# Kernel tuning notes

Hardware: AMD Instinct MI355X
Metric: run time of the kernel (lower is better)

Reference implementation:

```python
import jax, jax.numpy as jnp
import numpy as np

B, S, IN_DIM, HID, H, CS = 4, 4096, 1024, 1024, 16, 16
HD = HID // H
LN_EPS = 1e-5


def setup_inputs() -> dict:
    key = jax.random.key(0)
    ks = jax.random.split(key, 6)
    x = jax.random.normal(ks[0], (B, S, IN_DIM), jnp.float32)
    W_in = jax.random.normal(ks[1], (HID, IN_DIM), jnp.float32) * (IN_DIM ** -0.5)
    ln_g = jnp.ones((HID,), jnp.float32)
    ln_b = jnp.zeros((HID,), jnp.float32)
    W_gate = jax.random.normal(ks[2], (2 * H, HID), jnp.float32) * (HID ** -0.5)
    b_gate = jnp.zeros((2 * H,), jnp.float32)
    raw = 0.5 * float(np.log(1.9 / 0.1))  # atanh(0.9), as in _init_eigenvalues
    eig_raw = jnp.full((H,), raw, jnp.float32) + 0.01 * jax.random.normal(ks[3], (H,), jnp.float32)
    W_out = jax.random.normal(ks[4], (HID, HID), jnp.float32) * (HID ** -0.5)
    return {"x": x, "W_in": W_in, "ln_g": ln_g, "ln_b": ln_b,
            "W_gate": W_gate, "b_gate": b_gate, "eig_raw": eig_raw, "W_out": W_out}


def _chunk_scan(a, b):
    # a: (B,S,H) decay, b: (B,S,H,HD) input; h_t = a_t*h_{t-1} + b_t, h0 = 0
    Bsz, Sl = a.shape[0], a.shape[1]
    N = Sl // CS  # seq_len chosen divisible by chunk_size (pad_len == 0)
    ac = a.reshape(Bsz, N, CS, H)
    bc = b.reshape(Bsz, N, CS, H, HD)
    cum = jnp.cumprod(ac, axis=2)  # (B,N,C,H)
    ones = jnp.ones((Bsz, N, 1, H), a.dtype)
    cum_pad = jnp.concatenate([ones, cum[:, :, :-1]], axis=2)  # shifted cumprod
    # M[i,j] = cum_i / cum_pad_j for i>j, 1 on diag, 0 above
    Mi = cum[:, :, :, None, :]        # (B,N,C,1,H)
    Mj = cum_pad[:, :, None, :, :]    # (B,N,1,C,H)
    M = jnp.where(jnp.abs(Mj) > 1e-8, Mi / Mj, jnp.zeros_like(Mi))
    tril = jnp.tril(jnp.ones((CS, CS), a.dtype))[None, None, :, :, None]
    eye = jnp.eye(CS, dtype=a.dtype)[None, None, :, :, None]
    M = M * tril
    M = M * (1 - eye) + eye  # force exact 1 on diagonal
    # within-chunk contribution: (B,N,C,H,HD)
    h_contrib = jnp.einsum('bnijh,bnjhd->bnihd', M, bc)
    # inter-chunk sequential carry
    cum_T = jnp.moveaxis(cum, 1, 0)            # (N,B,C,H)
    hc_T = jnp.moveaxis(h_contrib, 1, 0)       # (N,B,C,H,HD)

    def step(h, inp):
        cum_n, hc_n = inp
        h_chunk = cum_n[..., None] * h[:, None] + hc_n  # (B,C,H,HD)
        return h_chunk[:, -1], h_chunk

    h0 = jnp.zeros((Bsz, H, HD), a.dtype)
    _, h_all = jax.lax.scan(step, h0, (cum_T, hc_T))   # (N,B,C,H,HD)
    h_all = jnp.moveaxis(h_all, 0, 1).reshape(Bsz, Sl, HID)
    return h_all


def reference(x, W_in, ln_g, ln_b, W_gate, b_gate, eig_raw, W_out):
    Bsz, Sl, _ = x.shape
    xp = x @ W_in.T                               # (B,S,HID)
    mu = jnp.mean(xp, axis=-1, keepdims=True)
    var = jnp.mean((xp - mu) ** 2, axis=-1, keepdims=True)
    xp = (xp - mu) * jax.lax.rsqrt(var + LN_EPS) * ln_g + ln_b
    gates = xp @ W_gate.T + b_gate                # (B,S,2H)
    alpha = jax.nn.sigmoid(gates[..., :H])
    beta = jax.nn.sigmoid(gates[..., H:])
    eig = jnp.tanh(eig_raw)                       # (H,)
    a = eig[None, None, :] * alpha                # (B,S,H)
    x_heads = xp.reshape(Bsz, Sl, H, HD)
    b = beta[..., None] * x_heads                 # (B,S,H,HD)
    h_all = _chunk_scan(a, b)                     # (B,S,HID)
    output = h_all @ W_out.T                      # dropout is identity in eval
    h_final = h_all[:, -1, :]
    return output, h_final
```

## Files before the change

kernel.cpp:

```cpp
#include <hip/hip_runtime.h>
#include <hip/hip_bf16.h>
#include <stdint.h>

#define BATCH 4
#define SEQ   4096
#define HID   1024
#define NH    16
#define HD    64
#define CS    16
#define NCH   256
#define MROWS 16384

typedef __attribute__((ext_vector_type(8))) __bf16 bf16x8;
typedef __attribute__((ext_vector_type(4))) float  f32x4;

__device__ __forceinline__ unsigned short f2bf(float f) {
    union { float f; unsigned u; } x; x.f = f;
    unsigned r = x.u + 0x7FFFu + ((x.u >> 16) & 1u);
    return (unsigned short)(r >> 16);
}
__device__ __forceinline__ float bf2f(unsigned short v) {
    union { unsigned u; float f; } x; x.u = ((unsigned)v) << 16;
    return x.f;
}

__device__ __forceinline__ void async_copy16(void* lds, const void* g) {
    __builtin_amdgcn_global_load_lds(
        (const __attribute__((address_space(1))) unsigned int*)g,
        (__attribute__((address_space(3))) unsigned int*)lds,
        16, 0, 0);
}

__global__ __launch_bounds__(256) void convert_all_kernel(
    const float* __restrict__ x, const float* __restrict__ W_in,
    const float* __restrict__ W_out, const float* __restrict__ W_gate,
    unsigned short* __restrict__ xb, unsigned short* __restrict__ Wib,
    unsigned short* __restrict__ Wob, unsigned short* __restrict__ Wgb)
{
    int i = blockIdx.x * 256 + threadIdx.x;
    const float4* src; ushort4* dst; int j;
    if (i < 4194304)      { src = (const float4*)x;      dst = (ushort4*)xb;  j = i; }
    else if (i < 4456448) { src = (const float4*)W_in;   dst = (ushort4*)Wib; j = i - 4194304; }
    else if (i < 4718592) { src = (const float4*)W_out;  dst = (ushort4*)Wob; j = i - 4456448; }
    else if (i < 4726784) { src = (const float4*)W_gate; dst = (ushort4*)Wgb; j = i - 4718592; }
    else return;
    float4 v = src[j];
    ushort4 o;
    o.x = f2bf(v.x); o.y = f2bf(v.y); o.z = f2bf(v.z); o.w = f2bf(v.w);
    dst[j] = o;
}

__global__ __launch_bounds__(256, 2) void gemm_bt_kernel(
    const unsigned short* __restrict__ A,
    const unsigned short* __restrict__ Bm,
    float* __restrict__ C, int M, int N, int K)
{
    __shared__ unsigned short As[128 * 64];
    __shared__ unsigned short Bs[128 * 64];
    const int t = threadIdx.x;
    const int lane = t & 63, w = t >> 6;
    const int wm = w >> 1, wn = w & 1;
    const size_t bm = (size_t)blockIdx.x * 128;
    const size_t bn = (size_t)blockIdx.y * 128;

    f32x4 acc[4][4];
#pragma unroll
    for (int x = 0; x < 4; x++)
#pragma unroll
        for (int y = 0; y < 4; y++)
            acc[x][y] = (f32x4){0.f, 0.f, 0.f, 0.f};

    const int srow = lane >> 3;
    const int gc   = (lane & 7) ^ (srow & 7);
    const int scol = gc * 8;
    const unsigned short* Ag = A + (bm + w * 32 + srow) * (size_t)K + scol;
    const unsigned short* Bg = Bm + (bn + w * 32 + srow) * (size_t)K + scol;
    unsigned short* Al = As + (w * 32 + srow) * 64 + (lane & 7) * 8;
    unsigned short* Bl = Bs + (w * 32 + srow) * 64 + (lane & 7) * 8;

    const int fr = lane & 15, fq = lane >> 4;
    const int rl = fr & 7;

    for (int k0 = 0; k0 < K; k0 += 64) {
#pragma unroll
        for (int r = 0; r < 4; r++) {
            async_copy16(Al + r * 8 * 64, Ag + (size_t)r * 8 * K + k0);
            async_copy16(Bl + r * 8 * 64, Bg + (size_t)r * 8 * K + k0);
        }
        __syncthreads();
#pragma unroll
        for (int kk = 0; kk < 64; kk += 32) {
            const int c = (kk >> 3) + fq;
            const int pc = c ^ rl;
            bf16x8 af[4], bfv[4];
#pragma unroll
            for (int x = 0; x < 4; x++) {
                af[x]  = *(const bf16x8*)(As + (wm * 64 + x * 16 + fr) * 64 + pc * 8);
                bfv[x] = *(const bf16x8*)(Bs + (wn * 64 + x * 16 + fr) * 64 + pc * 8);
            }
#pragma unroll
            for (int x = 0; x < 4; x++)
#pragma unroll
                for (int y = 0; y < 4; y++)
                    acc[x][y] = __builtin_amdgcn_mfma_f32_16x16x32_bf16(af[x], bfv[y], acc[x][y], 0, 0, 0);
        }
        __syncthreads();
    }

#pragma unroll
    for (int x = 0; x < 4; x++) {
#pragma unroll
        for (int y = 0; y < 4; y++) {
            size_t r0 = bm + wm * 64 + x * 16 + fq * 4;
            size_t c  = bn + wn * 64 + y * 16 + fr;
#pragma unroll
            for (int rg = 0; rg < 4; rg++)
                C[(r0 + rg) * (size_t)N + c] = acc[x][y][rg];
        }
    }
}

__global__ __launch_bounds__(256) void mid_kernel(
    const float* __restrict__ xp,
    const float* __restrict__ ln_g, const float* __restrict__ ln_b,
    const unsigned short* __restrict__ Wgb,
    const float* __restrict__ bg, const float* __restrict__ eig_raw,
    unsigned short* __restrict__ xln,
    float* __restrict__ beta_buf,
    float* __restrict__ cum_out,
    float* __restrict__ c15c,
    float* __restrict__ hc15)
{
    __shared__ unsigned short sx[16][1032];
    __shared__ float red[4][2][64][4];
    __shared__ float sg[16][32];
    __shared__ float scum[16][16];
    const int t = threadIdx.x, lane = t & 63, w = t >> 6;
    const int bn = blockIdx.x;
    const size_t m0 = (size_t)(bn >> 8) * SEQ + (size_t)(bn & 255) * 16;

    const int r = t >> 4, u = t & 15;
    {
        const float* row = xp + (m0 + r) * 1024;
        float4 v[16];
        float s = 0.f, s2 = 0.f;
#pragma unroll
        for (int i = 0; i < 16; i++) {
            v[i] = *(const float4*)(row + u * 4 + i * 64);
            s  += v[i].x + v[i].y + v[i].z + v[i].w;
            s2 += v[i].x * v[i].x + v[i].y * v[i].y + v[i].z * v[i].z + v[i].w * v[i].w;
        }
#pragma unroll
        for (int off = 1; off < 16; off <<= 1) {
            s  += __shfl_xor(s, off, 64);
            s2 += __shfl_xor(s2, off, 64);
        }
        const float mu = s * (1.f / 1024.f);
        const float var = s2 * (1.f / 1024.f) - mu * mu;
        const float sc = rsqrtf(var + 1e-5f);
        unsigned short* orow = xln + (m0 + r) * 1024;
#pragma unroll
        for (int i = 0; i < 16; i++) {
            const int k = u * 4 + i * 64;
            float4 g4 = *(const float4*)(ln_g + k);
            float4 b4 = *(const float4*)(ln_b + k);
            ushort4 o;
            o.x = f2bf((v[i].x - mu) * sc * g4.x + b4.x);
            o.y = f2bf((v[i].y - mu) * sc * g4.y + b4.y);
            o.z = f2bf((v[i].z - mu) * sc * g4.z + b4.z);
            o.w = f2bf((v[i].w - mu) * sc * g4.w + b4.w);
            *(ushort4*)&sx[r][k] = o;
            *(ushort4*)(orow + k) = o;
        }
    }
    __syncthreads();

    const int fr = lane & 15, fq = lane >> 4;
    {
        f32x4 acc0 = (f32x4){0.f,0.f,0.f,0.f}, acc1 = (f32x4){0.f,0.f,0.f,0.f};
        const unsigned short* Wr0 = Wgb + (size_t)fr * 1024;
        const unsigned short* Wr1 = Wgb + (size_t)(16 + fr) * 1024;
#pragma unroll
        for (int ks = 0; ks < 8; ks++) {
            const int k0 = w * 256 + ks * 32 + fq * 8;
            bf16x8 af = *(const bf16x8*)&sx[fr][k0];
            bf16x8 b0 = *(const bf16x8*)(Wr0 + k0);
            bf16x8 b1 = *(const bf16x8*)(Wr1 + k0);
            acc0 = __builtin_amdgcn_mfma_f32_16x16x32_bf16(af, b0, acc0, 0, 0, 0);
            acc1 = __builtin_amdgcn_mfma_f32_16x16x32_bf16(af, b1, acc1, 0, 0, 0);
        }
        *(f32x4*)&red[w][0][lane][0] = acc0;
        *(f32x4*)&red[w][1][lane][0] = acc1;
    }
    __syncthreads();
    if (t < 128) {
        const int y = t >> 6, l = t & 63;
        f32x4 s = *(const f32x4*)&red[0][y][l][0];
#pragma unroll
        for (int ww = 1; ww < 4; ww++) {
            f32x4 p = *(const f32x4*)&red[ww][y][l][0];
            s[0] += p[0]; s[1] += p[1]; s[2] += p[2]; s[3] += p[3];
        }
        const int col = y * 16 + (l & 15);
        const int row0 = (l >> 4) * 4;
        const float bias = bg[col];
#pragma unroll
        for (int rg = 0; rg < 4; rg++)
            sg[row0 + rg][col] = 1.f / (1.f + expf(-(s[rg] + bias)));
    }
    __syncthreads();

    if (t < 16) {
        const float ev = tanhf(eig_raw[t]);
        float c = 1.f;
#pragma unroll
        for (int i = 0; i < 16; i++) { c *= ev * sg[i][t]; scum[i][t] = c; }
    }
    beta_buf[(m0 + r) * 16 + u] = sg[r][16 + u];
    __syncthreads();

    cum_out[(size_t)bn * 256 + t] = scum[t >> 4][t & 15];
    if (t < 16) c15c[bn * 16 + t] = scum[15][t];

    {
        const int h = t >> 4, d0 = (t & 15) * 4;
        float s0 = 0.f, s1 = 0.f, s2 = 0.f, s3 = 0.f;
        float b0 = 0.f, b1 = 0.f, b2 = 0.f, b3 = 0.f;
        float cprev = 1.f;
#pragma unroll
        for (int j = 0; j < 16; j++) {
            const float bt = sg[j][16 + h];
            ushort4 xv = *(const ushort4*)&sx[j][h * 64 + d0];
            b0 = bt * bf2f(xv.x); b1 = bt * bf2f(xv.y);
            b2 = bt * bf2f(xv.z); b3 = bt * bf2f(xv.w);
            if (j < 15) {
                const float inv = (fabsf(cprev) > 1e-8f) ? (1.f / cprev) : 0.f;
                s0 += b0 * inv; s1 += b1 * inv; s2 += b2 * inv; s3 += b3 * inv;
                cprev = scum[j][h];
            }
        }
        const float c15 = scum[15][h];
        float4 o = { c15 * s0 + b0, c15 * s1 + b1, c15 * s2 + b2, c15 * s3 + b3 };
        *(float4*)(hc15 + (size_t)bn * 1024 + h * 64 + d0) = o;
    }
}

__global__ __launch_bounds__(64) void scan2_kernel(
    const float* __restrict__ c15c,
    const float* __restrict__ hc15,
    float* __restrict__ carry_in,
    float* __restrict__ h_final)
{
    const int p = blockIdx.x * 64 + threadIdx.x;
    const int b = p >> 10, hd = p & 1023, h = hd >> 6;
    float carry = 0.f;
#pragma unroll 8
    for (int n = 0; n < NCH; n++) {
        const size_t bn = (size_t)b * NCH + n;
        const float c15 = c15c[bn * 16 + h];
        carry_in[bn * 1024 + hd] = carry;
        carry = c15 * carry + hc15[bn * 1024 + hd];
    }
    h_final[(size_t)b * 1024 + hd] = carry;
}

__global__ __launch_bounds__(256) void scan3_kernel(
    const float* __restrict__ cum_buf,
    const float* __restrict__ beta_buf,
    const unsigned short* __restrict__ xln,
    const float* __restrict__ carry_in,
    unsigned short* __restrict__ hall)
{
    __shared__ float scum[16][16];
    __shared__ float sbeta[16][16];
    const int t = threadIdx.x;
    const int bn = blockIdx.x;
    const size_t m0 = (size_t)(bn >> 8) * SEQ + (size_t)(bn & 255) * 16;

    scum[t >> 4][t & 15]  = cum_buf[(size_t)bn * 256 + t];
    sbeta[t >> 4][t & 15] = beta_buf[(m0 + (t >> 4)) * 16 + (t & 15)];
    __syncthreads();

    const int h = t >> 4, dq = t & 15;
    const size_t off = h * 64 + dq * 4;
    float4 s = *(const float4*)(carry_in + (size_t)bn * 1024 + off);
    float cprev = 1.f;
#pragma unroll
    for (int i = 0; i < 16; i++) {
        ushort4 xv = *(const ushort4*)(xln + (m0 + i) * 1024 + off);
        const float bt = sbeta[i][h];
        const float b0 = bt * bf2f(xv.x), b1 = bt * bf2f(xv.y),
                    b2 = bt * bf2f(xv.z), b3 = bt * bf2f(xv.w);
        const float ci = scum[i][h];
        ushort4 o;
        o.x = f2bf(ci * s.x + b0); o.y = f2bf(ci * s.y + b1);
        o.z = f2bf(ci * s.z + b2); o.w = f2bf(ci * s.w + b3);
        *(ushort4*)(hall + (m0 + i) * 1024 + off) = o;
        const float inv = (fabsf(cprev) > 1e-8f) ? (1.f / cprev) : 0.f;
        s.x += b0 * inv; s.y += b1 * inv; s.z += b2 * inv; s.w += b3 * inv;
        cprev = ci;
    }
}

extern "C" void kernel_launch(void* const* d_in, const int* in_sizes, int n_in,
                              void* d_out, int out_size, void* d_ws, size_t ws_size,
                              hipStream_t stream)
{
    const float* x       = (const float*)d_in[0];
    const float* W_in    = (const float*)d_in[1];
    const float* ln_g    = (const float*)d_in[2];
    const float* ln_b    = (const float*)d_in[3];
    const float* W_gate  = (const float*)d_in[4];
    const float* b_gate  = (const float*)d_in[5];
    const float* eig_raw = (const float*)d_in[6];
    const float* W_out   = (const float*)d_in[7];
    float* out = (float*)d_out;

    char* ws = (char*)d_ws;
    unsigned short* xb   = (unsigned short*)(ws);
    unsigned short* xln  = (unsigned short*)(ws);
    unsigned short* hall = (unsigned short*)(ws + 33554432);
    unsigned short* Wib  = (unsigned short*)(ws + 67108864);
    unsigned short* Wob  = (unsigned short*)(ws + 69206016);
    unsigned short* Wgb  = (unsigned short*)(ws + 71303168);
    float* beta_buf = (float*)(ws + 71368704);
    float* cum_buf  = (float*)(ws + 72417280);
    float* c15c     = (float*)(ws + 73465856);
    float* hc15     = (float*)(ws + 73531392);
    float* carry_in = (float*)(ws + 77725696);

    float* xp = out;
    float* h_final = out + 16777216;

    convert_all_kernel<<<18464, 256, 0, stream>>>(x, W_in, W_out, W_gate, xb, Wib, Wob, Wgb);

    dim3 gg(128, 8);
    gemm_bt_kernel<<<gg, 256, 0, stream>>>(xb, Wib, xp, MROWS, HID, HID);

    mid_kernel<<<1024, 256, 0, stream>>>(xp, ln_g, ln_b, Wgb, b_gate, eig_raw,
                                         xln, beta_buf, cum_buf, c15c, hc15);

    scan2_kernel<<<64, 64, 0, stream>>>(c15c, hc15, carry_in, h_final);
    scan3_kernel<<<1024, 256, 0, stream>>>(cum_buf, beta_buf, xln, carry_in, hall);

    gemm_bt_kernel<<<gg, 256, 0, stream>>>(hall, Wob, out, MROWS, HID, HID);
}
```

Baseline: 265.5 us.

## Replace GEMM with 256x256 double-buffered tile kernel and interleaved staging

The 128x128 single-buffered bf16 GEMM is replaced by a 256x256-tile, 512-thread kernel. It double-buffers LDS, interleaves async global-to-LDS copies for the next K tile with MFMA work on the current one, raises wave priority around MFMA blocks, and remaps block IDs for L2 locality. The aim is to hide load latency behind compute and raise operand reuse per block in both projection GEMMs. The cost is 128KB of LDS per block and many barriers, and a 256-block grid gives about one block per CU, which may limit occupancy and latency hiding.

```diff
diff --git a/kernel.cpp b/kernel.cpp
--- a/kernel.cpp
+++ b/kernel.cpp
@@ -30,6 +30,9 @@
         (__attribute__((address_space(3))) unsigned int*)lds,
         16, 0, 0);
 }
+
+#define FENCE() asm volatile("" ::: "memory")
+#define BARRIER() do { FENCE(); __builtin_amdgcn_s_barrier(); FENCE(); } while (0)
 
 __global__ __launch_bounds__(256) void convert_all_kernel(
     const float* __restrict__ x, const float* __restrict__ W_in,
@@ -50,69 +53,141 @@
     dst[j] = o;
 }
 
-__global__ __launch_bounds__(256, 2) void gemm_bt_kernel(
+#define GBM 256
+#define GBN 256
+#define GBK 64
+
+__global__ __launch_bounds__(512, 2) void gemm256_kernel(
     const unsigned short* __restrict__ A,
     const unsigned short* __restrict__ Bm,
     float* __restrict__ C, int M, int N, int K)
 {
-    __shared__ unsigned short As[128 * 64];
-    __shared__ unsigned short Bs[128 * 64];
+    __shared__ unsigned short As[2][GBM][GBK];
+    __shared__ unsigned short Bs[2][GBN][GBK];
+
     const int t = threadIdx.x;
     const int lane = t & 63, w = t >> 6;
-    const int wm = w >> 1, wn = w & 1;
-    const size_t bm = (size_t)blockIdx.x * 128;
-    const size_t bn = (size_t)blockIdx.y * 128;
-
-    f32x4 acc[4][4];
-#pragma unroll
-    for (int x = 0; x < 4; x++)
+    const int wm = w >> 2, wn = w & 3;
+
+    const int nwg = gridDim.x;
+    const int cpx = nwg >> 3;
+    const int bid = blockIdx.x;
+    const int swz = (bid & 7) * cpx + (bid >> 3);
+    const int ntile = N >> 8;
+    const size_t bm = (size_t)(swz / ntile) * GBM;
+    const size_t bn = (size_t)(swz % ntile) * GBN;
+
+    const int srow = t >> 3;
+    const int sp   = t & 7;
+    const int sgc  = sp ^ (srow & 7);
+    const unsigned short* Ag = A  + (bm + srow) * (size_t)K + sgc * 8;
+    const unsigned short* Bg = Bm + (bn + srow) * (size_t)K + sgc * 8;
+
+    const int fr = lane & 15, fq = lane >> 4;
+    const int frl = fr & 7;
+
+    f32x4 acc[8][4];
+#pragma unroll
+    for (int x = 0; x < 8; x++)
 #pragma unroll
         for (int y = 0; y < 4; y++)
             acc[x][y] = (f32x4){0.f, 0.f, 0.f, 0.f};
 
-    const int srow = lane >> 3;
-    const int gc   = (lane & 7) ^ (srow & 7);
-    const int scol = gc * 8;
-    const unsigned short* Ag = A + (bm + w * 32 + srow) * (size_t)K + scol;
-    const unsigned short* Bg = Bm + (bn + w * 32 + srow) * (size_t)K + scol;
-    unsigned short* Al = As + (w * 32 + srow) * 64 + (lane & 7) * 8;
-    unsigned short* Bl = Bs + (w * 32 + srow) * 64 + (lane & 7) * 8;
-
-    const int fr = lane & 15, fq = lane >> 4;
-    const int rl = fr & 7;
-
-    for (int k0 = 0; k0 < K; k0 += 64) {
-#pragma unroll
-        for (int r = 0; r < 4; r++) {
-            async_copy16(Al + r * 8 * 64, Ag + (size_t)r * 8 * K + k0);
-            async_copy16(Bl + r * 8 * 64, Bg + (size_t)r * 8 * K + k0);
-        }
-        __syncthreads();
-#pragma unroll
-        for (int kk = 0; kk < 64; kk += 32) {
-            const int c = (kk >> 3) + fq;
-            const int pc = c ^ rl;
-            bf16x8 af[4], bfv[4];
-#pragma unroll
-            for (int x = 0; x < 4; x++) {
-                af[x]  = *(const bf16x8*)(As + (wm * 64 + x * 16 + fr) * 64 + pc * 8);
-                bfv[x] = *(const bf16x8*)(Bs + (wn * 64 + x * 16 + fr) * 64 + pc * 8);
-            }
+    bf16x8 afr[4][2];
+    bf16x8 bf0[2][2];
+    bf16x8 bf1[2][2];
+
+    auto stage = [&](int par, int h, int k0) {
+        if (h < 2) {
+            const unsigned short* g = Ag + ((size_t)h * 128) * K + k0;
+            unsigned short* l = &As[par][h * 128 + srow][sp * 8];
+            async_copy16(l,            g);
+            async_copy16(l + 64 * GBK, g + (size_t)64 * K);
+        } else {
+            const int hh = h - 2;
+            const unsigned short* g = Bg + ((size_t)hh * 128) * K + k0;
+            unsigned short* l = &Bs[par][hh * 128 + srow][sp * 8];
+            async_copy16(l,            g);
+            async_copy16(l + 64 * GBK, g + (size_t)64 * K);
+        }
+    };
+    auto rdA = [&](int par, int xh) {
+#pragma unroll
+        for (int x = 0; x < 4; x++)
+#pragma unroll
+            for (int kk = 0; kk < 2; kk++)
+                afr[x][kk] = *(const bf16x8*)&As[par][wm * 128 + xh * 64 + x * 16 + fr]
+                                                    [((kk * 4 + fq) ^ frl) * 8];
+    };
+    auto rdB = [&](int par, int yh, bf16x8 (&bfv)[2][2]) {
+#pragma unroll
+        for (int y = 0; y < 2; y++)
+#pragma unroll
+            for (int kk = 0; kk < 2; kk++)
+                bfv[y][kk] = *(const bf16x8*)&Bs[par][wn * 64 + yh * 32 + y * 16 + fr]
+                                                    [((kk * 4 + fq) ^ frl) * 8];
+    };
+    auto mm = [&](bf16x8 (&bfv)[2][2], int x0, int y0) {
+        __builtin_amdgcn_s_setprio(1);
+#pragma unroll
+        for (int kk = 0; kk < 2; kk++)
 #pragma unroll
             for (int x = 0; x < 4; x++)
 #pragma unroll
-                for (int y = 0; y < 4; y++)
-                    acc[x][y] = __builtin_amdgcn_mfma_f32_16x16x32_bf16(af[x], bfv[y], acc[x][y], 0, 0, 0);
-        }
-        __syncthreads();
-    }
-
-#pragma unroll
-    for (int x = 0; x < 4; x++) {
+                for (int y = 0; y < 2; y++)
+                    acc[x0 + x][y0 + y] = __builtin_amdgcn_mfma_f32_16x16x32_bf16(
+                        afr[x][kk], bfv[y][kk], acc[x0 + x][y0 + y], 0, 0, 0);
+        __builtin_amdgcn_s_setprio(0);
+    };
+
+    const int NT = K >> 6;
+
+#pragma unroll
+    for (int h = 0; h < 4; h++) stage(0, h, 0);
+    asm volatile("s_waitcnt vmcnt(0)" ::: "memory");
+    BARRIER();
+
+    int par = 0;
+    for (int tt = 0; tt < NT - 1; ++tt, par ^= 1) {
+        const int k1 = (tt + 1) << 6;
+        stage(par ^ 1, 0, k1);
+        asm volatile("s_waitcnt vmcnt(2)" ::: "memory");
+        BARRIER();
+        rdA(par, 0); rdB(par, 0, bf0);
+        mm(bf0, 0, 0);
+        BARRIER();
+        rdB(par, 1, bf1);
+        stage(par ^ 1, 1, k1);
+        BARRIER();
+        mm(bf1, 0, 2);
+        BARRIER();
+        rdA(par, 1);
+        stage(par ^ 1, 2, k1);
+        BARRIER();
+        mm(bf0, 4, 0);
+        BARRIER();
+        stage(par ^ 1, 3, k1);
+        BARRIER();
+        mm(bf1, 4, 2);
+        BARRIER();
+    }
+
+    asm volatile("s_waitcnt vmcnt(0)" ::: "memory");
+    BARRIER();
+    rdA(par, 0); rdB(par, 0, bf0);
+    mm(bf0, 0, 0);
+    rdB(par, 1, bf1);
+    mm(bf1, 0, 2);
+    rdA(par, 1);
+    mm(bf0, 4, 0);
+    mm(bf1, 4, 2);
+
+#pragma unroll
+    for (int x = 0; x < 8; x++) {
 #pragma unroll
         for (int y = 0; y < 4; y++) {
-            size_t r0 = bm + wm * 64 + x * 16 + fq * 4;
-            size_t c  = bn + wn * 64 + y * 16 + fr;
+            const size_t r0 = bm + wm * 128 + x * 16 + fq * 4;
+            const size_t c  = bn + wn * 64 + y * 16 + fr;
 #pragma unroll
             for (int rg = 0; rg < 4; rg++)
                 C[(r0 + rg) * (size_t)N + c] = acc[x][y][rg];
@@ -334,8 +409,7 @@
 
     convert_all_kernel<<<18464, 256, 0, stream>>>(x, W_in, W_out, W_gate, xb, Wib, Wob, Wgb);
 
-    dim3 gg(128, 8);
-    gemm_bt_kernel<<<gg, 256, 0, stream>>>(xb, Wib, xp, MROWS, HID, HID);
+    gemm256_kernel<<<256, 512, 0, stream>>>(xb, Wib, xp, MROWS, HID, HID);
 
     mid_kernel<<<1024, 256, 0, stream>>>(xp, ln_g, ln_b, Wgb, b_gate, eig_raw,
                                          xln, beta_buf, cum_buf, c15c, hc15);
@@ -343,5 +417,5 @@
     scan2_kernel<<<64, 64, 0, stream>>>(c15c, hc15, carry_in, h_final);
     scan3_kernel<<<1024, 256, 0, stream>>>(cum_buf, beta_buf, xln, carry_in, hall);
 
-    gemm_bt_kernel<<<gg, 256, 0, stream>>>(hall, Wob, out, MROWS, HID, HID);
-}
+    gemm256_kernel<<<256, 512, 0, stream>>>(hall, Wob, out, MROWS, HID, HID);
+}
```

After: 264.4 us. About the same (-0.4%).

## Parallelize inter-chunk carry scan into three-phase blocked scan

Applied to the files above, without the earlier changes.

Replaces the single sequential inter-chunk carry kernel, which ran 256 dependent steps with only 4096 threads, by a three-phase blocked scan. Phase one reduces groups of 16 chunks into a (product, sum) pair, phase two scans the 16 groups, and phase three rescans each group from its group carry. The aim is to cut the serial latency of the carry chain and expose more parallelism. The cost is two extra launches and a second read of hc15. The scratch buffers reuse the hall region, which scan3 only writes after these kernels finish.

```diff
diff --git a/kernel.cpp b/kernel.cpp
--- a/kernel.cpp
+++ b/kernel.cpp
@@ -245,23 +245,58 @@
     }
 }
 
-__global__ __launch_bounds__(64) void scan2_kernel(
+__global__ __launch_bounds__(256) void scan2a_kernel(
     const float* __restrict__ c15c,
     const float* __restrict__ hc15,
-    float* __restrict__ carry_in,
+    float* __restrict__ Pg,
+    float* __restrict__ Sg)
+{
+    const int tid = blockIdx.x * 256 + threadIdx.x;
+    const int b = tid >> 14, g = (tid >> 10) & 15, hd = tid & 1023, h = hd >> 6;
+    const int n0 = b * NCH + g * 16;
+    float P = 1.f, S = 0.f;
+#pragma unroll
+    for (int j = 0; j < 16; j++) {
+        const float c = c15c[(n0 + j) * 16 + h];
+        S = c * S + hc15[(size_t)(n0 + j) * 1024 + hd];
+        P = c * P;
+    }
+    Pg[tid] = P;
+    Sg[tid] = S;
+}
+
+__global__ __launch_bounds__(64) void scan2b_kernel(
+    const float* __restrict__ Pg, const float* __restrict__ Sg,
+    float* __restrict__ GC,
     float* __restrict__ h_final)
 {
     const int p = blockIdx.x * 64 + threadIdx.x;
-    const int b = p >> 10, hd = p & 1023, h = hd >> 6;
-    float carry = 0.f;
-#pragma unroll 8
-    for (int n = 0; n < NCH; n++) {
-        const size_t bn = (size_t)b * NCH + n;
-        const float c15 = c15c[bn * 16 + h];
-        carry_in[bn * 1024 + hd] = carry;
-        carry = c15 * carry + hc15[bn * 1024 + hd];
-    }
-    h_final[(size_t)b * 1024 + hd] = carry;
+    const int b = p >> 10, hd = p & 1023;
+    float gc = 0.f;
+#pragma unroll
+    for (int g = 0; g < 16; g++) {
+        const int idx = (b * 16 + g) * 1024 + hd;
+        GC[idx] = gc;
+        gc = Pg[idx] * gc + Sg[idx];
+    }
+    h_final[p] = gc;
+}
+
+__global__ __launch_bounds__(256) void scan2c_kernel(
+    const float* __restrict__ c15c, const float* __restrict__ hc15,
+    const float* __restrict__ GC,
+    float* __restrict__ carry_in)
+{
+    const int tid = blockIdx.x * 256 + threadIdx.x;
+    const int b = tid >> 14, g = (tid >> 10) & 15, hd = tid & 1023, h = hd >> 6;
+    const int n0 = b * NCH + g * 16;
+    float s = GC[tid];
+#pragma unroll
+    for (int j = 0; j < 16; j++) {
+        const size_t bn = n0 + j;
+        carry_in[bn * 1024 + hd] = s;
+        s = c15c[bn * 16 + h] * s + hc15[bn * 1024 + hd];
+    }
 }
 
 __global__ __launch_bounds__(256) void scan3_kernel(
@@ -329,6 +364,10 @@
     float* hc15     = (float*)(ws + 73531392);
     float* carry_in = (float*)(ws + 77725696);
 
+    float* Pg = (float*)(ws + 33554432);
+    float* Sg = (float*)(ws + 33554432 + 262144);
+    float* GC = (float*)(ws + 33554432 + 524288);
+
     float* xp = out;
     float* h_final = out + 16777216;
 
@@ -340,7 +379,10 @@
     mid_kernel<<<1024, 256, 0, stream>>>(xp, ln_g, ln_b, Wgb, b_gate, eig_raw,
                                          xln, beta_buf, cum_buf, c15c, hc15);
 
-    scan2_kernel<<<64, 64, 0, stream>>>(c15c, hc15, carry_in, h_final);
+    scan2a_kernel<<<256, 256, 0, stream>>>(c15c, hc15, Pg, Sg);
+    scan2b_kernel<<<64, 64, 0, stream>>>(Pg, Sg, GC, h_final);
+    scan2c_kernel<<<256, 256, 0, stream>>>(c15c, hc15, GC, carry_in);
+
     scan3_kernel<<<1024, 256, 0, stream>>>(cum_buf, beta_buf, xln, carry_in, hall);
 
     gemm_bt_kernel<<<gg, 256, 0, stream>>>(hall, Wob, out, MROWS, HID, HID);
```

After: 255.3 us. -3.8%, faster.
